# Performance work log

Hardware: AMD Instinct MI355X
Metric: run time of the kernel (lower is better)

Reference implementation:

```python
import jax, jax.numpy as jnp
import numpy as np

B, T, E = 16, 1024, 1024
G, N, D = 4, 8, 128
V = 2048


def setup_inputs() -> dict:
    key = jax.random.key(0)
    k1, k2, k3, k4 = jax.random.split(key, 4)
    x_emb = jax.random.normal(k1, (B, T, E), dtype=jnp.float32)
    W_in = jax.random.normal(k2, (E, G * N * D), dtype=jnp.float32) / np.sqrt(E)
    R = jax.random.normal(k3, (G, N, D, D), dtype=jnp.float32) / np.sqrt(D)
    b = jnp.zeros((G, N, D), dtype=jnp.float32)
    W_proj = jax.random.normal(k4, (V, N * D), dtype=jnp.float32) / np.sqrt(D)
    b_proj = jnp.zeros((V,), dtype=jnp.float32)
    return {"x_emb": x_emb, "W_in": W_in, "R": R, "b": b, "W_proj": W_proj, "b_proj": b_proj}


def reference(x_emb, W_in, R, b, W_proj, b_proj):
    # Input projection for all timesteps at once: [B,T,G,N,D]
    Bx, Tx, Ex = x_emb.shape
    Wx = jnp.einsum('bte,eg->btg', x_emb, W_in).reshape(Bx, Tx, G, N, D)

    def step(carry, wx_t):
        h, c = carry  # [B,N,D] each
        # per-head matrix recurrence: R[g] @ h  -> [B,G,N,D]
        gates = wx_t + jnp.einsum('gnde,bne->bgnd', R, h) + b
        i = jax.nn.sigmoid(gates[:, 0])
        f = jax.nn.sigmoid(gates[:, 1])
        z = jnp.tanh(gates[:, 2])
        o = jax.nn.sigmoid(gates[:, 3])
        c_new = f * c + i * z
        h_new = o * jnp.tanh(c_new)
        return (h_new, c_new), h_new

    h0 = jnp.zeros((Bx, N, D), dtype=x_emb.dtype)
    c0 = jnp.zeros((Bx, N, D), dtype=x_emb.dtype)
    (hN, cN), hs = jax.lax.scan(step, (h0, c0), jnp.swapaxes(Wx, 0, 1))  # hs: [T,B,N,D]
    h_flat = jnp.swapaxes(hs, 0, 1).reshape(Bx, Tx, N * D)
    logits = jnp.einsum('btn,vn->btv', h_flat, W_proj) + b_proj
    return logits
```

## Files before the change

### kernel.cpp

```cpp
#include <hip/hip_runtime.h>
#include <hip/hip_bf16.h>

#define DEV __device__ __forceinline__

using bf16 = __hip_bfloat16;
typedef __attribute__((ext_vector_type(8))) short short8v;
typedef __attribute__((ext_vector_type(4))) float f32x4;

constexpr int Bq = 16, Tq = 1024, Eq = 1024, Gq = 4, Nq = 8, Dq = 128, Vq = 2048;
constexpr int M1 = Bq * Tq;
constexpr int N1q = Gq * Nq * Dq;
constexpr int K1 = Eq;
constexpr int K2 = Nq * Dq;
constexpr int N2 = Vq;

DEV unsigned short bfu(float x) {
  union { bf16 h; unsigned short u; } cv;
  cv.h = __float2bfloat16(x);
  return cv.u;
}

DEV float rcp_(float x) { return __builtin_amdgcn_rcpf(x); }
DEV float sigm(float x) { return rcp_(1.0f + __expf(-x)); }
DEV float tanh_(float x) { return fmaf(2.0f, rcp_(1.0f + __expf(-2.0f * x)), -1.0f); }

#define GLD16(gp, lp)                                                       \
  __builtin_amdgcn_global_load_lds(                                        \
      (const __attribute__((address_space(1))) void*)(gp),                 \
      (__attribute__((address_space(3))) void*)(lp), 16, 0, 0)

__global__ __launch_bounds__(256) void cast_f32_bf16(const float* __restrict__ s,
                                                     bf16* __restrict__ d, int n4) {
  const int i = blockIdx.x * 256 + threadIdx.x;
  if (i >= n4) return;
  const float4 v = ((const float4*)s)[i];
  ushort4 u;
  u.x = bfu(v.x); u.y = bfu(v.y); u.z = bfu(v.z); u.w = bfu(v.w);
  ((ushort4*)d)[i] = u;
}

__global__ __launch_bounds__(256) void transpose_cast(const float* __restrict__ s,
                                                      bf16* __restrict__ d,
                                                      int SK, int SN) {
  __shared__ float t[32][33];
  const int n0 = blockIdx.x * 32, k0 = blockIdx.y * 32;
  const int tx = threadIdx.x & 31, ty = threadIdx.x >> 5;
#pragma unroll
  for (int i = 0; i < 32; i += 8)
    t[ty + i][tx] = s[(size_t)(k0 + ty + i) * SN + n0 + tx];
  __syncthreads();
#pragma unroll
  for (int i = 0; i < 32; i += 8)
    d[(size_t)(n0 + ty + i) * SK + k0 + tx] = __float2bfloat16(t[tx][ty + i]);
}

template <bool BF16_OUT, bool ADD_BIAS>
__global__ __launch_bounds__(256) void gemm_bt(const bf16* __restrict__ A,
                                               const bf16* __restrict__ Bt,
                                               void* __restrict__ Cout,
                                               const float* __restrict__ bp,
                                               int K, int N) {
  __shared__ bf16 As[128 * 32];
  __shared__ bf16 Bs[128 * 32];
  const int m0 = blockIdx.y * 128, n0 = blockIdx.x * 128;
  const int tid = threadIdx.x;
  const int lane = tid & 63, w = tid >> 6;
  const int wm = w >> 1, wn = w & 1;

  const int srow = lane >> 2, scol = (lane & 3) * 8;
  const int ca = w * 2;
  const bf16* Ag0 = A + (size_t)(m0 + ca * 16 + srow) * K + scol;
  const bf16* Ag1 = Ag0 + (size_t)16 * K;
  const bf16* Bg0 = Bt + (size_t)(n0 + ca * 16 + srow) * K + scol;
  const bf16* Bg1 = Bg0 + (size_t)16 * K;
  bf16* Al0 = As + ca * 512;
  bf16* Al1 = Al0 + 512;
  bf16* Bl0 = Bs + ca * 512;
  bf16* Bl1 = Bl0 + 512;

  f32x4 acc[4][4] = {};

  const int rr = lane & 15;
  const int kb = (lane >> 4) * 8;

  for (int k0 = 0; k0 < K; k0 += 32) {
    GLD16(Ag0 + k0, Al0);
    GLD16(Ag1 + k0, Al1);
    GLD16(Bg0 + k0, Bl0);
    GLD16(Bg1 + k0, Bl1);
    __syncthreads();
    short8v af[4], bfr[4];
#pragma unroll
    for (int i = 0; i < 4; ++i) {
      af[i]  = *(const short8v*)&As[(wm * 64 + i * 16 + rr) * 32 + kb];
      bfr[i] = *(const short8v*)&Bs[(wn * 64 + i * 16 + rr) * 32 + kb];
    }
#pragma unroll
    for (int i = 0; i < 4; ++i)
#pragma unroll
      for (int j = 0; j < 4; ++j)
        acc[i][j] = __builtin_amdgcn_mfma_f32_16x16x32_bf16(af[i], bfr[j], acc[i][j], 0, 0, 0);
    __syncthreads();
  }

  const int crow = (lane >> 4) * 4, ccol = lane & 15;
  if constexpr (BF16_OUT) {
    bf16* C = (bf16*)Cout;
#pragma unroll
    for (int i = 0; i < 4; ++i)
#pragma unroll
      for (int j = 0; j < 4; ++j) {
        const size_t base =
            (size_t)(m0 + wm * 64 + i * 16 + crow) * N + (n0 + wn * 64 + j * 16 + ccol);
#pragma unroll
        for (int jj = 0; jj < 4; ++jj)
          C[base + (size_t)jj * N] = __float2bfloat16(acc[i][j][jj]);
      }
  } else {
    float* C = (float*)Cout;
    float bv[4];
#pragma unroll
    for (int j = 0; j < 4; ++j)
      bv[j] = ADD_BIAS ? bp[n0 + wn * 64 + j * 16 + ccol] : 0.f;
#pragma unroll
    for (int i = 0; i < 4; ++i)
#pragma unroll
      for (int j = 0; j < 4; ++j) {
        const size_t base =
            (size_t)(m0 + wm * 64 + i * 16 + crow) * N + (n0 + wn * 64 + j * 16 + ccol);
#pragma unroll
        for (int jj = 0; jj < 4; ++jj)
          C[base + (size_t)jj * N] = acc[i][j][jj] + bv[j];
      }
  }
}

__global__ __launch_bounds__(512) void lstm_mfma(const bf16* __restrict__ Wx,
                                                 const float* __restrict__ R,
                                                 const float* __restrict__ bias,
                                                 bf16* __restrict__ h_all) {
  const int wg = blockIdx.x;
  const int bb = wg >> 3;
  const int n = wg & 7;
  const int tid = threadIdx.x;
  const int w = tid >> 6, lane = tid & 63;
  const int lg = lane >> 4;
  const int lc = lane & 15;
  const int d = w * 16 + lc;

  short8v Bf[4][4];
#pragma unroll
  for (int g = 0; g < 4; ++g)
#pragma unroll
    for (int kf = 0; kf < 4; ++kf) {
      const float* rp = R + (size_t)((g * Nq + n) * Dq + d) * Dq + 32 * kf + 8 * lg;
      const float4 r0 = *(const float4*)rp;
      const float4 r1 = *(const float4*)(rp + 4);
      short8v bv;
      bv[0] = (short)bfu(r0.x); bv[1] = (short)bfu(r0.y);
      bv[2] = (short)bfu(r0.z); bv[3] = (short)bfu(r0.w);
      bv[4] = (short)bfu(r1.x); bv[5] = (short)bfu(r1.y);
      bv[6] = (short)bfu(r1.z); bv[7] = (short)bfu(r1.w);
      Bf[g][kf] = bv;
    }

  float bvf[4];
#pragma unroll
  for (int g = 0; g < 4; ++g) bvf[g] = bias[(g * Nq + n) * Dq + d];

  __shared__ __align__(16) bf16 hbuf[2][128];
  if (tid < 128) hbuf[0][tid] = __float2bfloat16(0.f);
  __syncthreads();

  const bf16* wx0 = Wx + (size_t)bb * Tq * 4096 + n * Dq + d;
  bf16* hallp = h_all + ((size_t)(bb * Tq) * Nq + n) * Dq + d;

  bf16 wxr[4][4];
#pragma unroll
  for (int u = 0; u < 4; ++u)
#pragma unroll
    for (int g = 0; g < 4; ++g) wxr[u][g] = wx0[(size_t)u * 4096 + g * 1024];

  float c = 0.f;

  for (int t0 = 0; t0 < Tq; t0 += 4) {
#pragma unroll
    for (int u = 0; u < 4; ++u) {
      const int t = t0 + u;
      const bf16* hb = hbuf[t & 1];
      short8v Af[4];
#pragma unroll
      for (int kf = 0; kf < 4; ++kf)
        Af[kf] = *(const short8v*)(hb + 32 * kf + 8 * lg);

      f32x4 accA[4], accB[4];
#pragma unroll
      for (int g = 0; g < 4; ++g) {
        const float pre = __bfloat162float(wxr[u][g]) + bvf[g];
        accA[g][0] = pre; accA[g][1] = pre; accA[g][2] = pre; accA[g][3] = pre;
        accB[g][0] = 0.f; accB[g][1] = 0.f; accB[g][2] = 0.f; accB[g][3] = 0.f;
      }
#pragma unroll
      for (int g = 0; g < 4; ++g) {
        accA[g] = __builtin_amdgcn_mfma_f32_16x16x32_bf16(Af[0], Bf[g][0], accA[g], 0, 0, 0);
        accB[g] = __builtin_amdgcn_mfma_f32_16x16x32_bf16(Af[2], Bf[g][2], accB[g], 0, 0, 0);
        accA[g] = __builtin_amdgcn_mfma_f32_16x16x32_bf16(Af[1], Bf[g][1], accA[g], 0, 0, 0);
        accB[g] = __builtin_amdgcn_mfma_f32_16x16x32_bf16(Af[3], Bf[g][3], accB[g], 0, 0, 0);
      }

      {
        const int tp = (t + 4 < Tq) ? (t + 4) : (Tq - 1);
#pragma unroll
        for (int g = 0; g < 4; ++g) wxr[u][g] = wx0[(size_t)tp * 4096 + g * 1024];
      }

      const float i_ = sigm(accA[0][0] + accB[0][0]);
      const float f_ = sigm(accA[1][0] + accB[1][0]);
      const float z_ = tanh_(accA[2][0] + accB[2][0]);
      const float o_ = sigm(accA[3][0] + accB[3][0]);
      c = f_ * c + i_ * z_;
      const float h = o_ * tanh_(c);
      const bf16 h16 = __float2bfloat16(h);

      if (lg == 0) {
        hbuf[(t + 1) & 1][d] = h16;
        hallp[(size_t)t * (Nq * Dq)] = h16;
      }
      __builtin_amdgcn_sched_barrier(0);
      asm volatile("s_waitcnt lgkmcnt(0)" ::: "memory");
      __builtin_amdgcn_sched_barrier(0);
      __builtin_amdgcn_s_barrier();
      __builtin_amdgcn_sched_barrier(0);
    }
  }
}

extern "C" void kernel_launch(void* const* d_in, const int* in_sizes, int n_in,
                              void* d_out, int out_size, void* d_ws, size_t ws_size,
                              hipStream_t stream) {
  const float* x_emb = (const float*)d_in[0];
  const float* W_in  = (const float*)d_in[1];
  const float* R     = (const float*)d_in[2];
  const float* bias  = (const float*)d_in[3];
  const float* W_prj = (const float*)d_in[4];
  const float* b_prj = (const float*)d_in[5];

  char* ws = (char*)d_ws;
  bf16* xb  = (bf16*)ws;
  bf16* WiT = (bf16*)(ws + (size_t)M1 * K1 * 2);
  bf16* Wpb = WiT + (size_t)N1q * K1;
  bf16* H   = Wpb + (size_t)N2 * K2;
  bf16* Wx = (bf16*)d_out;

  cast_f32_bf16<<<(M1 * K1 / 4 + 255) / 256, 256, 0, stream>>>(x_emb, xb, M1 * K1 / 4);
  transpose_cast<<<dim3(N1q / 32, K1 / 32), 256, 0, stream>>>(W_in, WiT, K1, N1q);
  cast_f32_bf16<<<(N2 * K2 / 4 + 255) / 256, 256, 0, stream>>>(W_prj, Wpb, N2 * K2 / 4);

  gemm_bt<true, false><<<dim3(N1q / 128, M1 / 128), 256, 0, stream>>>(
      xb, WiT, (void*)Wx, nullptr, K1, N1q);

  lstm_mfma<<<dim3(Bq * Nq), 512, 0, stream>>>(Wx, R, bias, H);

  gemm_bt<false, true><<<dim3(N2 / 128, M1 / 128), 256, 0, stream>>>(
      H, Wpb, d_out, b_prj, K2, N2);
}
```

Baseline: 803.3 us.

## Store Wx gate-interleaved per (b,n) stream and split MFMA accumulation chains

The input-projection GEMM now writes Wx in a [b][n][t][d][g] layout, so each LSTM thread loads its four gate preactivations with one 8-byte load from a contiguous per-(b,n) stream instead of four scattered 2-byte loads. The recurrence also splits its MFMA accumulation into four independent chains instead of two, to shorten the dependent MFMA latency on the serial per-timestep path. The cost is a scattered, uncoalesced 2-byte store pattern in the GEMM epilogue.

Result: slower. 829.7 us (+3.3%).

```diff
diff --git a/kernel.cpp b/kernel.cpp
--- a/kernel.cpp
+++ b/kernel.cpp
@@ -54,7 +54,7 @@
     d[(size_t)(n0 + ty + i) * SK + k0 + tx] = __float2bfloat16(t[tx][ty + i]);
 }
 
-template <bool BF16_OUT, bool ADD_BIAS>
+template <int MODE>
 __global__ __launch_bounds__(256) void gemm_bt(const bf16* __restrict__ A,
                                                const bf16* __restrict__ Bt,
                                                void* __restrict__ Cout,
@@ -104,24 +104,27 @@
   }
 
   const int crow = (lane >> 4) * 4, ccol = lane & 15;
-  if constexpr (BF16_OUT) {
+  if constexpr (MODE == 2) {
     bf16* C = (bf16*)Cout;
 #pragma unroll
     for (int i = 0; i < 4; ++i)
 #pragma unroll
       for (int j = 0; j < 4; ++j) {
-        const size_t base =
-            (size_t)(m0 + wm * 64 + i * 16 + crow) * N + (n0 + wn * 64 + j * 16 + ccol);
-#pragma unroll
-        for (int jj = 0; jj < 4; ++jj)
-          C[base + (size_t)jj * N] = __float2bfloat16(acc[i][j][jj]);
+        const int col = n0 + wn * 64 + j * 16 + ccol;
+        const int g = col >> 10, nn = (col >> 7) & 7, dd = col & 127;
+#pragma unroll
+        for (int jj = 0; jj < 4; ++jj) {
+          const int row = m0 + wm * 64 + i * 16 + crow + jj;
+          const int b = row >> 10, t = row & 1023;
+          C[(((size_t)(b * 8 + nn) * 1024 + t) << 9) + dd * 4 + g] =
+              __float2bfloat16(acc[i][j][jj]);
+        }
       }
   } else {
     float* C = (float*)Cout;
     float bv[4];
 #pragma unroll
-    for (int j = 0; j < 4; ++j)
-      bv[j] = ADD_BIAS ? bp[n0 + wn * 64 + j * 16 + ccol] : 0.f;
+    for (int j = 0; j < 4; ++j) bv[j] = bp[n0 + wn * 64 + j * 16 + ccol];
 #pragma unroll
     for (int i = 0; i < 4; ++i)
 #pragma unroll
@@ -172,14 +175,13 @@
   if (tid < 128) hbuf[0][tid] = __float2bfloat16(0.f);
   __syncthreads();
 
-  const bf16* wx0 = Wx + (size_t)bb * Tq * 4096 + n * Dq + d;
+  const bf16* wx0 = Wx + ((size_t)(bb * 8 + n) << 19) + d * 4;
   bf16* hallp = h_all + ((size_t)(bb * Tq) * Nq + n) * Dq + d;
 
-  bf16 wxr[4][4];
+  ushort4 wxr[4];
 #pragma unroll
   for (int u = 0; u < 4; ++u)
-#pragma unroll
-    for (int g = 0; g < 4; ++g) wxr[u][g] = wx0[(size_t)u * 4096 + g * 1024];
+    wxr[u] = *(const ushort4*)(wx0 + ((size_t)u << 9));
 
   float c = 0.f;
 
@@ -193,31 +195,36 @@
       for (int kf = 0; kf < 4; ++kf)
         Af[kf] = *(const short8v*)(hb + 32 * kf + 8 * lg);
 
-      f32x4 accA[4], accB[4];
+      float wxf[4];
+      wxf[0] = __uint_as_float((unsigned)wxr[u].x << 16);
+      wxf[1] = __uint_as_float((unsigned)wxr[u].y << 16);
+      wxf[2] = __uint_as_float((unsigned)wxr[u].z << 16);
+      wxf[3] = __uint_as_float((unsigned)wxr[u].w << 16);
+
+      f32x4 a0[4], a1[4], a2[4], a3[4];
 #pragma unroll
       for (int g = 0; g < 4; ++g) {
-        const float pre = __bfloat162float(wxr[u][g]) + bvf[g];
-        accA[g][0] = pre; accA[g][1] = pre; accA[g][2] = pre; accA[g][3] = pre;
-        accB[g][0] = 0.f; accB[g][1] = 0.f; accB[g][2] = 0.f; accB[g][3] = 0.f;
+        const float pre = wxf[g] + bvf[g];
+        a0[g][0] = pre; a0[g][1] = pre; a0[g][2] = pre; a0[g][3] = pre;
+        a1[g] = {}; a2[g] = {}; a3[g] = {};
       }
 #pragma unroll
       for (int g = 0; g < 4; ++g) {
-        accA[g] = __builtin_amdgcn_mfma_f32_16x16x32_bf16(Af[0], Bf[g][0], accA[g], 0, 0, 0);
-        accB[g] = __builtin_amdgcn_mfma_f32_16x16x32_bf16(Af[2], Bf[g][2], accB[g], 0, 0, 0);
-        accA[g] = __builtin_amdgcn_mfma_f32_16x16x32_bf16(Af[1], Bf[g][1], accA[g], 0, 0, 0);
-        accB[g] = __builtin_amdgcn_mfma_f32_16x16x32_bf16(Af[3], Bf[g][3], accB[g], 0, 0, 0);
+        a0[g] = __builtin_amdgcn_mfma_f32_16x16x32_bf16(Af[0], Bf[g][0], a0[g], 0, 0, 0);
+        a1[g] = __builtin_amdgcn_mfma_f32_16x16x32_bf16(Af[1], Bf[g][1], a1[g], 0, 0, 0);
+        a2[g] = __builtin_amdgcn_mfma_f32_16x16x32_bf16(Af[2], Bf[g][2], a2[g], 0, 0, 0);
+        a3[g] = __builtin_amdgcn_mfma_f32_16x16x32_bf16(Af[3], Bf[g][3], a3[g], 0, 0, 0);
       }
 
       {
         const int tp = (t + 4 < Tq) ? (t + 4) : (Tq - 1);
-#pragma unroll
-        for (int g = 0; g < 4; ++g) wxr[u][g] = wx0[(size_t)tp * 4096 + g * 1024];
-      }
-
-      const float i_ = sigm(accA[0][0] + accB[0][0]);
-      const float f_ = sigm(accA[1][0] + accB[1][0]);
-      const float z_ = tanh_(accA[2][0] + accB[2][0]);
-      const float o_ = sigm(accA[3][0] + accB[3][0]);
+        wxr[u] = *(const ushort4*)(wx0 + ((size_t)tp << 9));
+      }
+
+      const float i_ = sigm((a0[0][0] + a1[0][0]) + (a2[0][0] + a3[0][0]));
+      const float f_ = sigm((a0[1][0] + a1[1][0]) + (a2[1][0] + a3[1][0]));
+      const float z_ = tanh_((a0[2][0] + a1[2][0]) + (a2[2][0] + a3[2][0]));
+      const float o_ = sigm((a0[3][0] + a1[3][0]) + (a2[3][0] + a3[3][0]));
       c = f_ * c + i_ * z_;
       const float h = o_ * tanh_(c);
       const bf16 h16 = __float2bfloat16(h);
@@ -256,11 +263,11 @@
   transpose_cast<<<dim3(N1q / 32, K1 / 32), 256, 0, stream>>>(W_in, WiT, K1, N1q);
   cast_f32_bf16<<<(N2 * K2 / 4 + 255) / 256, 256, 0, stream>>>(W_prj, Wpb, N2 * K2 / 4);
 
-  gemm_bt<true, false><<<dim3(N1q / 128, M1 / 128), 256, 0, stream>>>(
+  gemm_bt<2><<<dim3(N1q / 128, M1 / 128), 256, 0, stream>>>(
       xb, WiT, (void*)Wx, nullptr, K1, N1q);
 
   lstm_mfma<<<dim3(Bq * Nq), 512, 0, stream>>>(Wx, R, bias, H);
 
-  gemm_bt<false, true><<<dim3(N2 / 128, M1 / 128), 256, 0, stream>>>(
+  gemm_bt<0><<<dim3(N2 / 128, M1 / 128), 256, 0, stream>>>(
       H, Wpb, d_out, b_prj, K2, N2);
 }
```
